# Optimization experiments

Measured on AMD Instinct MI355X. Metric: run time of the kernel, lower is better.

The kernel has to match this reference:

```python
import jax, jax.numpy as jnp
import numpy as np

LN_EPS = 1e-5
SN_EPS = 1e-12


def _block(x, W, b, g, be):
    # Linear -> LayerNorm -> CELU, fused as one expression chain
    h = x @ W.T + b
    mu = jnp.mean(h, axis=-1, keepdims=True)
    var = jnp.mean(jnp.square(h - mu), axis=-1, keepdims=True)
    h = (h - mu) * jax.lax.rsqrt(var + LN_EPS) * g + be
    return jax.nn.celu(h)


def _spectral_norm_weight(W, u):
    # One power iteration (torch training-mode behavior), u/v detached.
    v = W.T @ u
    v = v / (jnp.linalg.norm(v) + SN_EPS)
    u2 = W @ v
    u2 = u2 / (jnp.linalg.norm(u2) + SN_EPS)
    sigma = u2 @ (W @ v)
    return W / sigma


def setup_inputs() -> dict:
    key = jax.random.key(0)
    ks = jax.random.split(key, 8)
    B, D = 131072, 512
    sizes = [512, 128, 32, 8]
    inp = {"x": jax.random.normal(ks[0], (B, D), dtype=jnp.float32)}
    fan_in = D
    for i, s in enumerate(sizes, start=1):
        scale = 1.0 / np.sqrt(fan_in)
        inp[f"W{i}"] = jax.random.normal(ks[i], (s, fan_in), dtype=jnp.float32) * scale
        inp[f"b{i}"] = jnp.zeros((s,), dtype=jnp.float32)
        inp[f"g{i}"] = jnp.ones((s,), dtype=jnp.float32)
        inp[f"be{i}"] = jnp.zeros((s,), dtype=jnp.float32)
        fan_in = s
    inp["Wh"] = jax.random.normal(ks[5], (1, 8), dtype=jnp.float32) * (1.0 / np.sqrt(8))
    inp["bh"] = jnp.zeros((1,), dtype=jnp.float32)
    inp["u"] = jax.random.normal(ks[6], (1,), dtype=jnp.float32)
    return inp


def reference(x, W1, b1, g1, be1, W2, b2, g2, be2, W3, b3, g3, be3,
              W4, b4, g4, be4, Wh, bh, u):
    h = _block(x, W1, b1, g1, be1)
    h = _block(h, W2, b2, g2, be2)
    h = _block(h, W3, b3, g3, be3)
    h = _block(h, W4, b4, g4, be4)          # hidden_output: [B, 8]
    Wsn = _spectral_norm_weight(Wh, u)
    return h @ Wsn.T + bh                   # [B, 1]
```

## Files before the change

kernel.cpp:

```cpp
#include <hip/hip_runtime.h>


typedef unsigned short u16;
typedef unsigned int   u32;
typedef __bf16  bf16x8 __attribute__((ext_vector_type(8)));
typedef float   f32x16 __attribute__((ext_vector_type(16)));

__device__ __forceinline__ u16 f2bf(float f) {
    u32 x = __builtin_bit_cast(u32, f);
    x += 0x7FFFu + ((x >> 16) & 1u);
    return (u16)(x >> 16);
}
__device__ __forceinline__ float bfval(u16 h) { return __builtin_bit_cast(float, (u32)h << 16); }
__device__ __forceinline__ u32 pack2(float a, float b) { return (u32)f2bf(a) | ((u32)f2bf(b) << 16); }
__device__ __forceinline__ float celu1(float x) { return x > 0.f ? x : __expf(x) - 1.f; }

#define W1F_OFF 0
#define W2F_OFF 262144
#define W3F_OFF 327680
#define W3LF_OFF 331776
#define NGROUPS 41984

__global__ void prep_weights(const float* __restrict__ W1, const float* __restrict__ W2,
                             const float* __restrict__ W3, u16* __restrict__ wsb) {
    const int g = blockIdx.x * 256 + threadIdx.x;
    if (g < 32768) {
        const int l = g & 63, t = (g >> 6) & 15, ksg = g >> 10;
        const int n = t * 32 + (l & 31);
        const int k0 = ksg * 16 + (l >> 5) * 8;
        u16* dst = wsb + W1F_OFF + g * 8;
        const float* src = W1 + n * 512 + k0;
#pragma unroll
        for (int e = 0; e < 8; ++e) dst[e] = f2bf(src[e]);
    } else if (g < 40960) {
        const int h = g - 32768;
        const int l = h & 63, t = (h >> 6) & 3, ksg = h >> 8;
        const int n = t * 32 + (l & 31);
        const int k0 = ksg * 16 + (l >> 5) * 8;
        u16* dst = wsb + W2F_OFF + h * 8;
        const float* src = W2 + n * 512 + k0;
#pragma unroll
        for (int e = 0; e < 8; ++e) dst[e] = f2bf(src[e]);
    } else if (g < 41472) {
        const int h = g - 40960;
        const int l = h & 63, ksg = h >> 6;
        const int n = l & 31;
        const int k0 = ksg * 16 + (l >> 5) * 8;
        u16* dst = wsb + W3F_OFF + h * 8;
        const float* src = W3 + n * 128 + k0;
#pragma unroll
        for (int e = 0; e < 8; ++e) dst[e] = f2bf(src[e]);
    } else {
        const int h = g - 41472;
        const int l = h & 63, ksg = h >> 6;
        const int n = l & 31;
        const int k0 = ksg * 16 + (l >> 5) * 8;
        u16* dst = wsb + W3LF_OFF + h * 8;
        const float* src = W3 + n * 128 + k0;
#pragma unroll
        for (int e = 0; e < 8; ++e) { float w = src[e]; dst[e] = f2bf(w - bfval(f2bf(w))); }
    }
}

#define PW4 0
#define PB4 256
#define PG4 264
#define PBE4 272
#define PWH 280
#define PBH 288
#define PU  289
#define NPAR 290

__global__ __launch_bounds__(512, 4) void fused_mlp(
    const float* __restrict__ x,
    const u16* __restrict__ W1b, const u16* __restrict__ W2b,
    const u16* __restrict__ W3b, const u16* __restrict__ W3Lb,
    const float* __restrict__ b1, const float* __restrict__ g1, const float* __restrict__ be1,
    const float* __restrict__ b2, const float* __restrict__ g2, const float* __restrict__ be2,
    const float* __restrict__ b3, const float* __restrict__ g3, const float* __restrict__ be3,
    const float* __restrict__ W4, const float* __restrict__ b4, const float* __restrict__ g4,
    const float* __restrict__ be4,
    const float* __restrict__ Wh, const float* __restrict__ bh, const float* __restrict__ uvec,
    float* __restrict__ out)
{
    __shared__ __align__(16) u16 sXH[64][520];
    __shared__ __align__(16) float sPS[64][8];
    __shared__ __align__(16) float sPQ[64][8];
    __shared__ __align__(8)  float2 sMR[64];
    __shared__ __align__(16) float sP[NPAR + 2];

    const int tid = threadIdx.x;
    const int wv = tid >> 6;
    const int lane = tid & 63;
    const int ln = lane & 31;
    const int lh = lane >> 5;
    const int Ng = wv;
    const int row0 = blockIdx.x * 64;

    const float b1a = b1[Ng * 64 + ln],  b1c = b1[Ng * 64 + 32 + ln];
    const float g1a = g1[Ng * 64 + ln],  g1c = g1[Ng * 64 + 32 + ln];
    const float e1a = be1[Ng * 64 + ln], e1c = be1[Ng * 64 + 32 + ln];
    const int Mt2 = wv >> 2, Nt2 = wv & 3;
    const float b2v = b2[Nt2 * 32 + ln], g2v = g2[Nt2 * 32 + ln], e2v = be2[Nt2 * 32 + ln];
    const float b3v = b3[ln], g3v = g3[ln], e3v = be3[ln];

    if (tid < NPAR) {
        float v;
        if      (tid < 256) v = W4[tid];
        else if (tid < 264) v = b4[tid - 256];
        else if (tid < 272) v = g4[tid - 264];
        else if (tid < 280) v = be4[tid - 272];
        else if (tid < 288) v = Wh[tid - 280];
        else if (tid == 288) v = bh[0];
        else                v = uvec[0];
        sP[tid] = v;
    }

    {
        const float4* xp = (const float4*)(x) + (long)blockIdx.x * 8192 + tid;
        float4 q[16];
#pragma unroll
        for (int j = 0; j < 16; ++j) q[j] = xp[j * 512];
        const int r0 = tid >> 7;
        const int c4 = (tid & 127) * 4;
#pragma unroll
        for (int j = 0; j < 16; ++j)
            *(uint2*)(&sXH[j * 4 + r0][c4]) =
                make_uint2(pack2(q[j].x, q[j].y), pack2(q[j].z, q[j].w));
    }
    __syncthreads();

    f32x16 acc[2][2] = {};
    {
        const u16* wq = W1b + (Ng * 2) * 512 + lane * 8;
        bf16x8 Bf[4][2];
#pragma unroll
        for (int s = 0; s < 3; ++s) {
            Bf[s][0] = *(const bf16x8*)(wq + s * 8192);
            Bf[s][1] = *(const bf16x8*)(wq + s * 8192 + 512);
        }
#pragma unroll
        for (int ksg = 0; ksg < 32; ++ksg) {
            const int slot = ksg & 3;
            if (ksg + 3 < 32) {
                const int ps = (ksg + 3) & 3;
                const u16* np = wq + (ksg + 3) * 8192;
                Bf[ps][0] = *(const bf16x8*)(np);
                Bf[ps][1] = *(const bf16x8*)(np + 512);
            }
            bf16x8 a0 = *(const bf16x8*)(&sXH[ln][ksg * 16 + lh * 8]);
            bf16x8 a1 = *(const bf16x8*)(&sXH[32 + ln][ksg * 16 + lh * 8]);
            acc[0][0] = __builtin_amdgcn_mfma_f32_32x32x16_bf16(a0, Bf[slot][0], acc[0][0], 0, 0, 0);
            acc[0][1] = __builtin_amdgcn_mfma_f32_32x32x16_bf16(a0, Bf[slot][1], acc[0][1], 0, 0, 0);
            acc[1][0] = __builtin_amdgcn_mfma_f32_32x32x16_bf16(a1, Bf[slot][0], acc[1][0], 0, 0, 0);
            acc[1][1] = __builtin_amdgcn_mfma_f32_32x32x16_bf16(a1, Bf[slot][1], acc[1][1], 0, 0, 0);
        }
    }

#pragma unroll
    for (int rg = 0; rg < 16; ++rg) {
        acc[0][0][rg] += b1a; acc[0][1][rg] += b1c;
        acc[1][0][rg] += b1a; acc[1][1][rg] += b1c;
    }
#pragma unroll
    for (int mt = 0; mt < 2; ++mt)
#pragma unroll
    for (int rg = 0; rg < 16; ++rg) {
        float s = acc[mt][0][rg] + acc[mt][1][rg];
        float q = acc[mt][0][rg] * acc[mt][0][rg] + acc[mt][1][rg] * acc[mt][1][rg];
#pragma unroll
        for (int m = 1; m < 32; m <<= 1) { s += __shfl_xor(s, m, 64); q += __shfl_xor(q, m, 64); }
        if (ln == 0) {
            const int row = mt * 32 + (rg & 3) + 8 * (rg >> 2) + 4 * lh;
            sPS[row][Ng] = s; sPQ[row][Ng] = q;
        }
    }
    __syncthreads();
    if (tid < 64) {
        float s = 0.f, q = 0.f;
#pragma unroll
        for (int j = 0; j < 8; ++j) { s += sPS[tid][j]; q += sPQ[tid][j]; }
        const float mu = s * (1.f / 512.f);
        const float var = q * (1.f / 512.f) - mu * mu;
        sMR[tid] = make_float2(mu, rsqrtf(var + 1e-5f));
    }
    __syncthreads();
#pragma unroll
    for (int mt = 0; mt < 2; ++mt)
#pragma unroll
    for (int rg = 0; rg < 16; ++rg) {
        const int row = mt * 32 + (rg & 3) + 8 * (rg >> 2) + 4 * lh;
        const float2 mr = sMR[row];
        const float h0 = (acc[mt][0][rg] - mr.x) * mr.y * g1a + e1a;
        const float h1v = (acc[mt][1][rg] - mr.x) * mr.y * g1c + e1c;
        sXH[row][Ng * 64 + ln] = f2bf(celu1(h0));
        sXH[row][Ng * 64 + 32 + ln] = f2bf(celu1(h1v));
    }
    __syncthreads();

    float v2[16];
    {
        const u16* w2q = W2b + Nt2 * 512 + lane * 8;
        bf16x8 W2f[4];
#pragma unroll
        for (int s = 0; s < 4; ++s) W2f[s] = *(const bf16x8*)(w2q + s * 2048);
        f32x16 a2 = {}, a2b = {};
        const u16* h1p = &sXH[Mt2 * 32 + ln][lh * 8];
#pragma unroll
        for (int ksg = 0; ksg < 32; ++ksg) {
            const int slot = ksg & 3;
            bf16x8 af = *(const bf16x8*)(h1p + ksg * 16);
            if (ksg & 1) a2b = __builtin_amdgcn_mfma_f32_32x32x16_bf16(af, W2f[slot], a2b, 0, 0, 0);
            else         a2  = __builtin_amdgcn_mfma_f32_32x32x16_bf16(af, W2f[slot], a2, 0, 0, 0);
            if (ksg + 4 < 32) W2f[slot] = *(const bf16x8*)(w2q + (ksg + 4) * 2048);
        }
#pragma unroll
        for (int rg = 0; rg < 16; ++rg) v2[rg] = a2[rg] + a2b[rg] + b2v;
#pragma unroll
        for (int rg = 0; rg < 16; ++rg) {
            float s = v2[rg], q = v2[rg] * v2[rg];
#pragma unroll
            for (int m = 1; m < 32; m <<= 1) { s += __shfl_xor(s, m, 64); q += __shfl_xor(q, m, 64); }
            if (ln == 0) {
                const int row = Mt2 * 32 + (rg & 3) + 8 * (rg >> 2) + 4 * lh;
                sPS[row][Nt2] = s; sPQ[row][Nt2] = q;
            }
        }
    }
    __syncthreads();
    if (tid < 64) {
        float s = sPS[tid][0] + sPS[tid][1] + sPS[tid][2] + sPS[tid][3];
        float q = sPQ[tid][0] + sPQ[tid][1] + sPQ[tid][2] + sPQ[tid][3];
        const float mu = s * (1.f / 128.f);
        const float var = q * (1.f / 128.f) - mu * mu;
        sMR[tid] = make_float2(mu, rsqrtf(var + 1e-5f));
    }
    __syncthreads();
    {
        const int col = Nt2 * 32 + ln;
#pragma unroll
        for (int rg = 0; rg < 16; ++rg) {
            const int row = Mt2 * 32 + (rg & 3) + 8 * (rg >> 2) + 4 * lh;
            const float2 mr = sMR[row];
            const float hn = (v2[rg] - mr.x) * mr.y * g2v + e2v;
            const float a = celu1(hn);
            const u16 hi = f2bf(a);
            sXH[row][col] = hi;
            sXH[row][128 + col] = f2bf(a - bfval(hi));
        }
    }
    __syncthreads();

    if (wv < 2) {
        f32x16 a3 = {};
        const u16* w3q  = W3b  + lane * 8;
        const u16* w3lq = W3Lb + lane * 8;
        const u16* h2p  = &sXH[wv * 32 + ln][lh * 8];
        const u16* h2lp = &sXH[wv * 32 + ln][128 + lh * 8];
#pragma unroll
        for (int ks = 0; ks < 8; ++ks) {
            bf16x8 fa_h = *(const bf16x8*)(h2p  + ks * 16);
            bf16x8 fa_l = *(const bf16x8*)(h2lp + ks * 16);
            bf16x8 fb_h = *(const bf16x8*)(w3q  + ks * 512);
            bf16x8 fb_l = *(const bf16x8*)(w3lq + ks * 512);
            a3 = __builtin_amdgcn_mfma_f32_32x32x16_bf16(fa_h, fb_h, a3, 0, 0, 0);
            a3 = __builtin_amdgcn_mfma_f32_32x32x16_bf16(fa_h, fb_l, a3, 0, 0, 0);
            a3 = __builtin_amdgcn_mfma_f32_32x32x16_bf16(fa_l, fb_h, a3, 0, 0, 0);
        }
#pragma unroll
        for (int rg = 0; rg < 16; ++rg) {
            const float v = a3[rg] + b3v;
            float s = v, q = v * v;
#pragma unroll
            for (int m = 1; m < 32; m <<= 1) { s += __shfl_xor(s, m, 64); q += __shfl_xor(q, m, 64); }
            const float mu = s * (1.f / 32.f);
            const float rs = rsqrtf(q * (1.f / 32.f) - mu * mu + 1e-5f);
            const int row = wv * 32 + (rg & 3) + 8 * (rg >> 2) + 4 * lh;
            float* s3 = (float*)&sXH[row][256 * 2];
            s3 = (float*)&sXH[row][0] + 128;
            s3[ln] = celu1((v - mu) * rs * g3v + e3v);
        }
    }
    __syncthreads();

    if (tid < 256) {
        const int r = tid & 63, og = tid >> 6;
        float h[32];
        const float4* hp = (const float4*)((float*)&sXH[r][0] + 128);
#pragma unroll
        for (int j = 0; j < 8; ++j) {
            float4 tv = hp[j];
            h[j * 4 + 0] = tv.x; h[j * 4 + 1] = tv.y; h[j * 4 + 2] = tv.z; h[j * 4 + 3] = tv.w;
        }
#pragma unroll
        for (int oo = 0; oo < 2; ++oo) {
            const int o = og * 2 + oo;
            float a = sP[PB4 + o];
            const float* w4 = &sP[PW4 + o * 32];
#pragma unroll
            for (int k = 0; k < 32; ++k) a += h[k] * w4[k];
            sPS[r][o] = a;
        }
    }
    __syncthreads();

    if (tid < 64) {
        float v[8];
        float s = 0.f, q = 0.f;
#pragma unroll
        for (int o = 0; o < 8; ++o) { v[o] = sPS[tid][o]; s += v[o]; q += v[o] * v[o]; }
        const float mu = s * 0.125f;
        const float var = q * 0.125f - mu * mu;
        const float rs = rsqrtf(var + 1e-5f);

        float wh[8];
        const float u0 = sP[PU];
        float nv = 0.f;
#pragma unroll
        for (int o = 0; o < 8; ++o) { wh[o] = sP[PWH + o]; float tt = wh[o] * u0; nv += tt * tt; }
        nv = sqrtf(nv);
        const float inv = 1.f / (nv + 1e-12f);
        float s2 = 0.f;
#pragma unroll
        for (int o = 0; o < 8; ++o) s2 += wh[o] * (wh[o] * u0 * inv);
        const float u2 = s2 / (fabsf(s2) + 1e-12f);
        const float sigma = u2 * s2;
        const float isg = 1.f / sigma;

        float y = sP[PBH];
#pragma unroll
        for (int o = 0; o < 8; ++o) {
            const float hn = (v[o] - mu) * rs * sP[PG4 + o] + sP[PBE4 + o];
            y += celu1(hn) * wh[o] * isg;
        }
        out[row0 + tid] = y;
    }
}

extern "C" void kernel_launch(void* const* d_in, const int* in_sizes, int n_in,
                              void* d_out, int out_size, void* d_ws, size_t ws_size,
                              hipStream_t stream) {
    const float* x   = (const float*)d_in[0];
    const float* W1  = (const float*)d_in[1];
    const float* b1  = (const float*)d_in[2];
    const float* g1  = (const float*)d_in[3];
    const float* be1 = (const float*)d_in[4];
    const float* W2  = (const float*)d_in[5];
    const float* b2  = (const float*)d_in[6];
    const float* g2  = (const float*)d_in[7];
    const float* be2 = (const float*)d_in[8];
    const float* W3  = (const float*)d_in[9];
    const float* b3  = (const float*)d_in[10];
    const float* g3  = (const float*)d_in[11];
    const float* be3 = (const float*)d_in[12];
    const float* W4  = (const float*)d_in[13];
    const float* b4  = (const float*)d_in[14];
    const float* g4  = (const float*)d_in[15];
    const float* be4 = (const float*)d_in[16];
    const float* Wh  = (const float*)d_in[17];
    const float* bh  = (const float*)d_in[18];
    const float* u   = (const float*)d_in[19];
    float* out = (float*)d_out;
    u16* wsb = (u16*)d_ws;

    prep_weights<<<dim3(NGROUPS / 256), dim3(256), 0, stream>>>(W1, W2, W3, wsb);

    const int rows = in_sizes[0] / 512;
    fused_mlp<<<dim3(rows / 64), dim3(512), 0, stream>>>(
        x, wsb + W1F_OFF, wsb + W2F_OFF, wsb + W3F_OFF, wsb + W3LF_OFF,
        b1, g1, be1, b2, g2, be2, b3, g3, be3,
        W4, b4, g4, be4, Wh, bh, u, out);
}
```

Before: 547.0 us.

## Halve rows per block from 64 to 32 to double block count

Each block now processes 32 rows instead of 64, which halves the shared-memory footprint and doubles the grid size. The layer-1 GEMM per wave drops to one M-tile, layer 2 runs on only four waves, and layer 3 on one. The aim is higher occupancy and more blocks to hide latency. In exchange, each W1 tile loaded from global/L2 is reused across half as many rows, doubling weight traffic per row, and more waves sit idle in the later layers.

```diff
diff --git a/kernel.cpp b/kernel.cpp
--- a/kernel.cpp
+++ b/kernel.cpp
@@ -83,10 +83,10 @@
     const float* __restrict__ Wh, const float* __restrict__ bh, const float* __restrict__ uvec,
     float* __restrict__ out)
 {
-    __shared__ __align__(16) u16 sXH[64][520];
-    __shared__ __align__(16) float sPS[64][8];
-    __shared__ __align__(16) float sPQ[64][8];
-    __shared__ __align__(8)  float2 sMR[64];
+    __shared__ __align__(16) u16 sXH[32][520];
+    __shared__ __align__(16) float sPS[32][8];
+    __shared__ __align__(16) float sPQ[32][8];
+    __shared__ __align__(8)  float2 sMR[32];
     __shared__ __align__(16) float sP[NPAR + 2];
 
     const int tid = threadIdx.x;
@@ -94,13 +94,12 @@
     const int lane = tid & 63;
     const int ln = lane & 31;
     const int lh = lane >> 5;
-    const int Ng = wv;
-    const int row0 = blockIdx.x * 64;
-
-    const float b1a = b1[Ng * 64 + ln],  b1c = b1[Ng * 64 + 32 + ln];
-    const float g1a = g1[Ng * 64 + ln],  g1c = g1[Ng * 64 + 32 + ln];
-    const float e1a = be1[Ng * 64 + ln], e1c = be1[Ng * 64 + 32 + ln];
-    const int Mt2 = wv >> 2, Nt2 = wv & 3;
+    const int row0 = blockIdx.x * 32;
+
+    const float b1a = b1[wv * 64 + ln],  b1c = b1[wv * 64 + 32 + ln];
+    const float g1a = g1[wv * 64 + ln],  g1c = g1[wv * 64 + 32 + ln];
+    const float e1a = be1[wv * 64 + ln], e1c = be1[wv * 64 + 32 + ln];
+    const int Nt2 = wv & 3;
     const float b2v = b2[Nt2 * 32 + ln], g2v = g2[Nt2 * 32 + ln], e2v = be2[Nt2 * 32 + ln];
     const float b3v = b3[ln], g3v = g3[ln], e3v = be3[ln];
 
@@ -117,22 +116,22 @@
     }
 
     {
-        const float4* xp = (const float4*)(x) + (long)blockIdx.x * 8192 + tid;
-        float4 q[16];
-#pragma unroll
-        for (int j = 0; j < 16; ++j) q[j] = xp[j * 512];
+        const float4* xp = (const float4*)(x) + (long)blockIdx.x * 4096 + tid;
+        float4 q[8];
+#pragma unroll
+        for (int j = 0; j < 8; ++j) q[j] = xp[j * 512];
         const int r0 = tid >> 7;
         const int c4 = (tid & 127) * 4;
 #pragma unroll
-        for (int j = 0; j < 16; ++j)
+        for (int j = 0; j < 8; ++j)
             *(uint2*)(&sXH[j * 4 + r0][c4]) =
                 make_uint2(pack2(q[j].x, q[j].y), pack2(q[j].z, q[j].w));
     }
     __syncthreads();
 
-    f32x16 acc[2][2] = {};
+    f32x16 acc[2] = {};
     {
-        const u16* wq = W1b + (Ng * 2) * 512 + lane * 8;
+        const u16* wq = W1b + (wv * 2) * 512 + lane * 8;
         bf16x8 Bf[4][2];
 #pragma unroll
         for (int s = 0; s < 3; ++s) {
@@ -149,34 +148,28 @@
                 Bf[ps][1] = *(const bf16x8*)(np + 512);
             }
             bf16x8 a0 = *(const bf16x8*)(&sXH[ln][ksg * 16 + lh * 8]);
-            bf16x8 a1 = *(const bf16x8*)(&sXH[32 + ln][ksg * 16 + lh * 8]);
-            acc[0][0] = __builtin_amdgcn_mfma_f32_32x32x16_bf16(a0, Bf[slot][0], acc[0][0], 0, 0, 0);
-            acc[0][1] = __builtin_amdgcn_mfma_f32_32x32x16_bf16(a0, Bf[slot][1], acc[0][1], 0, 0, 0);
-            acc[1][0] = __builtin_amdgcn_mfma_f32_32x32x16_bf16(a1, Bf[slot][0], acc[1][0], 0, 0, 0);
-            acc[1][1] = __builtin_amdgcn_mfma_f32_32x32x16_bf16(a1, Bf[slot][1], acc[1][1], 0, 0, 0);
+            acc[0] = __builtin_amdgcn_mfma_f32_32x32x16_bf16(a0, Bf[slot][0], acc[0], 0, 0, 0);
+            acc[1] = __builtin_amdgcn_mfma_f32_32x32x16_bf16(a0, Bf[slot][1], acc[1], 0, 0, 0);
         }
     }
 
 #pragma unroll
     for (int rg = 0; rg < 16; ++rg) {
-        acc[0][0][rg] += b1a; acc[0][1][rg] += b1c;
-        acc[1][0][rg] += b1a; acc[1][1][rg] += b1c;
-    }
-#pragma unroll
-    for (int mt = 0; mt < 2; ++mt)
+        acc[0][rg] += b1a; acc[1][rg] += b1c;
+    }
 #pragma unroll
     for (int rg = 0; rg < 16; ++rg) {
-        float s = acc[mt][0][rg] + acc[mt][1][rg];
-        float q = acc[mt][0][rg] * acc[mt][0][rg] + acc[mt][1][rg] * acc[mt][1][rg];
+        float s = acc[0][rg] + acc[1][rg];
+        float q = acc[0][rg] * acc[0][rg] + acc[1][rg] * acc[1][rg];
 #pragma unroll
         for (int m = 1; m < 32; m <<= 1) { s += __shfl_xor(s, m, 64); q += __shfl_xor(q, m, 64); }
         if (ln == 0) {
-            const int row = mt * 32 + (rg & 3) + 8 * (rg >> 2) + 4 * lh;
-            sPS[row][Ng] = s; sPQ[row][Ng] = q;
-        }
-    }
-    __syncthreads();
-    if (tid < 64) {
+            const int row = (rg & 3) + 8 * (rg >> 2) + 4 * lh;
+            sPS[row][wv] = s; sPQ[row][wv] = q;
+        }
+    }
+    __syncthreads();
+    if (tid < 32) {
         float s = 0.f, q = 0.f;
 #pragma unroll
         for (int j = 0; j < 8; ++j) { s += sPS[tid][j]; q += sPQ[tid][j]; }
@@ -186,26 +179,24 @@
     }
     __syncthreads();
 #pragma unroll
-    for (int mt = 0; mt < 2; ++mt)
-#pragma unroll
     for (int rg = 0; rg < 16; ++rg) {
-        const int row = mt * 32 + (rg & 3) + 8 * (rg >> 2) + 4 * lh;
+        const int row = (rg & 3) + 8 * (rg >> 2) + 4 * lh;
         const float2 mr = sMR[row];
-        const float h0 = (acc[mt][0][rg] - mr.x) * mr.y * g1a + e1a;
-        const float h1v = (acc[mt][1][rg] - mr.x) * mr.y * g1c + e1c;
-        sXH[row][Ng * 64 + ln] = f2bf(celu1(h0));
-        sXH[row][Ng * 64 + 32 + ln] = f2bf(celu1(h1v));
+        const float h0 = (acc[0][rg] - mr.x) * mr.y * g1a + e1a;
+        const float h1v = (acc[1][rg] - mr.x) * mr.y * g1c + e1c;
+        sXH[row][wv * 64 + ln] = f2bf(celu1(h0));
+        sXH[row][wv * 64 + 32 + ln] = f2bf(celu1(h1v));
     }
     __syncthreads();
 
     float v2[16];
-    {
+    if (wv < 4) {
         const u16* w2q = W2b + Nt2 * 512 + lane * 8;
         bf16x8 W2f[4];
 #pragma unroll
         for (int s = 0; s < 4; ++s) W2f[s] = *(const bf16x8*)(w2q + s * 2048);
         f32x16 a2 = {}, a2b = {};
-        const u16* h1p = &sXH[Mt2 * 32 + ln][lh * 8];
+        const u16* h1p = &sXH[ln][lh * 8];
 #pragma unroll
         for (int ksg = 0; ksg < 32; ++ksg) {
             const int slot = ksg & 3;
@@ -222,13 +213,13 @@
 #pragma unroll
             for (int m = 1; m < 32; m <<= 1) { s += __shfl_xor(s, m, 64); q += __shfl_xor(q, m, 64); }
             if (ln == 0) {
-                const int row = Mt2 * 32 + (rg & 3) + 8 * (rg >> 2) + 4 * lh;
+                const int row = (rg & 3) + 8 * (rg >> 2) + 4 * lh;
                 sPS[row][Nt2] = s; sPQ[row][Nt2] = q;
             }
         }
     }
     __syncthreads();
-    if (tid < 64) {
+    if (tid < 32) {
         float s = sPS[tid][0] + sPS[tid][1] + sPS[tid][2] + sPS[tid][3];
         float q = sPQ[tid][0] + sPQ[tid][1] + sPQ[tid][2] + sPQ[tid][3];
         const float mu = s * (1.f / 128.f);
@@ -236,11 +227,11 @@
         sMR[tid] = make_float2(mu, rsqrtf(var + 1e-5f));
     }
     __syncthreads();
-    {
+    if (wv < 4) {
         const int col = Nt2 * 32 + ln;
 #pragma unroll
         for (int rg = 0; rg < 16; ++rg) {
-            const int row = Mt2 * 32 + (rg & 3) + 8 * (rg >> 2) + 4 * lh;
+            const int row = (rg & 3) + 8 * (rg >> 2) + 4 * lh;
             const float2 mr = sMR[row];
             const float hn = (v2[rg] - mr.x) * mr.y * g2v + e2v;
             const float a = celu1(hn);
@@ -251,12 +242,12 @@
     }
     __syncthreads();
 
-    if (wv < 2) {
+    if (wv == 0) {
         f32x16 a3 = {};
         const u16* w3q  = W3b  + lane * 8;
         const u16* w3lq = W3Lb + lane * 8;
-        const u16* h2p  = &sXH[wv * 32 + ln][lh * 8];
-        const u16* h2lp = &sXH[wv * 32 + ln][128 + lh * 8];
+        const u16* h2p  = &sXH[ln][lh * 8];
+        const u16* h2lp = &sXH[ln][128 + lh * 8];
 #pragma unroll
         for (int ks = 0; ks < 8; ++ks) {
             bf16x8 fa_h = *(const bf16x8*)(h2p  + ks * 16);
@@ -275,36 +266,31 @@
             for (int m = 1; m < 32; m <<= 1) { s += __shfl_xor(s, m, 64); q += __shfl_xor(q, m, 64); }
             const float mu = s * (1.f / 32.f);
             const float rs = rsqrtf(q * (1.f / 32.f) - mu * mu + 1e-5f);
-            const int row = wv * 32 + (rg & 3) + 8 * (rg >> 2) + 4 * lh;
-            float* s3 = (float*)&sXH[row][256 * 2];
-            s3 = (float*)&sXH[row][0] + 128;
+            const int row = (rg & 3) + 8 * (rg >> 2) + 4 * lh;
+            float* s3 = (float*)&sXH[row][0] + 128;
             s3[ln] = celu1((v - mu) * rs * g3v + e3v);
         }
     }
     __syncthreads();
 
     if (tid < 256) {
-        const int r = tid & 63, og = tid >> 6;
+        const int r = tid & 31, o = tid >> 5;
         float h[32];
-        const float4* hp = (const float4*)((float*)&sXH[r][0] + 128);
+        const float4* hp = (const float4*)((const float*)&sXH[r][0] + 128);
 #pragma unroll
         for (int j = 0; j < 8; ++j) {
             float4 tv = hp[j];
             h[j * 4 + 0] = tv.x; h[j * 4 + 1] = tv.y; h[j * 4 + 2] = tv.z; h[j * 4 + 3] = tv.w;
         }
-#pragma unroll
-        for (int oo = 0; oo < 2; ++oo) {
-            const int o = og * 2 + oo;
-            float a = sP[PB4 + o];
-            const float* w4 = &sP[PW4 + o * 32];
-#pragma unroll
-            for (int k = 0; k < 32; ++k) a += h[k] * w4[k];
-            sPS[r][o] = a;
-        }
-    }
-    __syncthreads();
-
-    if (tid < 64) {
+        float a = sP[PB4 + o];
+        const float* w4 = &sP[PW4 + o * 32];
+#pragma unroll
+        for (int k = 0; k < 32; ++k) a += h[k] * w4[k];
+        sPS[r][o] = a;
+    }
+    __syncthreads();
+
+    if (tid < 32) {
         float v[8];
         float s = 0.f, q = 0.f;
 #pragma unroll
@@ -366,7 +352,7 @@
     prep_weights<<<dim3(NGROUPS / 256), dim3(256), 0, stream>>>(W1, W2, W3, wsb);
 
     const int rows = in_sizes[0] / 512;
-    fused_mlp<<<dim3(rows / 64), dim3(512), 0, stream>>>(
+    fused_mlp<<<dim3(rows / 32), dim3(512), 0, stream>>>(
         x, wsb + W1F_OFF, wsb + W2F_OFF, wsb + W3F_OFF, wsb + W3LF_OFF,
         b1, g1, be1, b2, g2, be2, b3, g3, be3,
         W4, b4, g4, be4, Wh, bh, u, out);
```

Result: slower. 595.6 us (+8.9%).
